# Performance work log

Measured on AMD Instinct MI355X. Metric: run time of the kernel, lower is better.

Reference implementation:

```python
import jax, jax.numpy as jnp
import numpy as np

B, F, A, U = 4096, 64, 8, 32  # batch, n_features, num_att, n_outputs
R = 2.0                       # the 'r' scaling inside exp(kernel * r)


def setup_inputs() -> dict:
    key = jax.random.key(0)
    k1, k2 = jax.random.split(key)
    inputs = jax.random.normal(k1, (B, F), dtype=jnp.float32)
    # per-exclusion-feature attention kernels, stacked: [F, A, F, U]
    limit = float(np.sqrt(6.0 / (F + U)))  # glorot_uniform
    kernels = jax.random.uniform(k2, (F, A, F, U), dtype=jnp.float32,
                                 minval=-limit, maxval=limit)
    return {"inputs": inputs, "kernels": kernels}


def reference(inputs, kernels):
    # inputs: [B, F]; kernels: [j=F excluded-feature index, A, F, U]
    f = inputs.shape[-1]
    mask = 1.0 - jnp.eye(f, dtype=inputs.dtype)          # [j, F]: zero out feature j
    xm = mask[:, None, :] * inputs[None, :, :]           # [j, B, F]
    z = jnp.einsum('jbf,jafu->jabu', xm, kernels)        # [j, A, B, U]
    z = jax.nn.softmax(z, axis=-1)                       # softmax over units
    w = jnp.exp(kernels * R)                             # [j, A, F, U]
    scores = jnp.einsum('jabu,jafu->jabf', z, w)         # [j, A, B, F]
    scores = scores.mean(axis=0)                         # mean over exclusion axis -> [A, B, F]
    return jax.nn.softmax(scores, axis=-1)               # [A, B, F]
```

## Files before the change

### kernel.cpp

```cpp
#include <hip/hip_runtime.h>
#include <hip/hip_bf16.h>
#include <math.h>

#define B_ 4096
#define F_ 64
#define A_ 8
#define U_ 32

typedef float f32x4 __attribute__((ext_vector_type(4)));
typedef short bf16x8 __attribute__((ext_vector_type(8)));

#define KD_OFF (4ull << 20)

static __device__ __forceinline__ unsigned int pk_bf16(float lo, float hi) {
    union { __hip_bfloat162 h2; unsigned int u; } cv;
    cv.h2 = __float22bfloat162_rn(make_float2(lo, hi));
    return cv.u;
}
static __device__ __forceinline__ float rb(float f) {
    unsigned int u = __float_as_uint(f);
    u += 0x7FFFu + ((u >> 16) & 1u);
    return __uint_as_float(u & 0xFFFF0000u);
}

__global__ __launch_bounds__(256) void ife_prep(const float* __restrict__ kern,
                                                unsigned char* __restrict__ ws)
{
    const int bid = blockIdx.x;
    const int a = bid >> 6, j = bid & 63;
    const int t = threadIdx.x;
    __shared__ float st[64][36];

    const float* src = kern + ((size_t)j * A_ + a) * (F_ * U_);
    {
        const int f = t >> 2, u0 = (t & 3) * 8;
        *(float4*)&st[f][u0]     = *(const float4*)&src[f * U_ + u0];
        *(float4*)&st[f][u0 + 4] = *(const float4*)&src[f * U_ + u0 + 4];
    }
    __syncthreads();

    unsigned char* dst = ws + (size_t)bid * 8192;
    const int fragid = t >> 6, lane = t & 63, q = lane >> 4, c = lane & 15;

    {
        const int kc = fragid >> 1, ut = fragid & 1;
        const int f0 = kc * 32 + q * 8, u = ut * 16 + c;
        unsigned int w[4];
        #pragma unroll
        for (int i = 0; i < 4; ++i)
            w[i] = pk_bf16(st[f0 + 2 * i][u], st[f0 + 2 * i + 1][u]);
        *(uint4*)(dst + fragid * 1024 + lane * 16) = make_uint4(w[0], w[1], w[2], w[3]);
    }
    {
        const int f = fragid * 16 + c, u0 = q * 8;
        const float4 wa = *(const float4*)&st[f][u0];
        const float4 wb = *(const float4*)&st[f][u0 + 4];
        unsigned int w[4];
        w[0] = pk_bf16(__expf(2.f * wa.x), __expf(2.f * wa.y));
        w[1] = pk_bf16(__expf(2.f * wa.z), __expf(2.f * wa.w));
        w[2] = pk_bf16(__expf(2.f * wb.x), __expf(2.f * wb.y));
        w[3] = pk_bf16(__expf(2.f * wb.z), __expf(2.f * wb.w));
        *(uint4*)(dst + 4096 + fragid * 1024 + lane * 16) = make_uint4(w[0], w[1], w[2], w[3]);
    }
    if (t < U_)
        ((float*)(ws + KD_OFF))[(size_t)bid * U_ + t] = rb(st[j][t]);
}

__global__ __launch_bounds__(256, 2) void ife_main(const float* __restrict__ x,
                                                   const unsigned char* __restrict__ ws,
                                                   float* __restrict__ out)
{
    const int a = blockIdx.y, bt = blockIdx.x, t = threadIdx.x;
    const int wv = t >> 6, lane = t & 63, q = lane >> 4, c = lane & 15;

    __shared__ float Xf[64][66];
    __shared__ float Kd[64][32];
    __shared__ __align__(16) unsigned int PbufA[4][16][20];
    __shared__ __align__(16) unsigned int PbufB[4][16][20];

    bf16x8 Xh[2];
    {
        const float* xr = x + (size_t)(bt * 64 + wv * 16 + c) * F_;
        #pragma unroll
        for (int kc = 0; kc < 2; ++kc) {
            const float4 va = *(const float4*)&xr[kc * 32 + q * 8];
            const float4 vb = *(const float4*)&xr[kc * 32 + q * 8 + 4];
            union { unsigned int u[4]; bf16x8 v; } H;
            H.u[0] = pk_bf16(va.x, va.y);
            H.u[1] = pk_bf16(va.z, va.w);
            H.u[2] = pk_bf16(vb.x, vb.y);
            H.u[3] = pk_bf16(vb.z, vb.w);
            Xh[kc] = H.v;
        }
    }
    {
        const int row = t >> 2, cb = (t & 3) * 16;
        const float* xsrc = x + (size_t)(bt * 64 + row) * F_ + cb;
        #pragma unroll
        for (int i = 0; i < 16; i += 4) {
            const float4 v = *(const float4*)&xsrc[i];
            Xf[row][cb + i]     = rb(v.x);
            Xf[row][cb + i + 1] = rb(v.y);
            Xf[row][cb + i + 2] = rb(v.z);
            Xf[row][cb + i + 3] = rb(v.w);
        }
    }
    {
        const float* kd = (const float*)(ws + KD_OFF) + (size_t)a * 64 * U_;
        const int jj = t >> 2, u0 = (t & 3) * 8;
        *(float4*)&Kd[jj][u0]     = *(const float4*)&kd[jj * U_ + u0];
        *(float4*)&Kd[jj][u0 + 4] = *(const float4*)&kd[jj * U_ + u0 + 4];
    }
    __syncthreads();

    const unsigned int psel = (q < 2) ? 0x05040100u : 0x07060302u;
    const unsigned char* fbase = ws + (size_t)a * 64 * 8192 + (size_t)lane * 16;

    union { unsigned int u[4]; bf16x8 v; } oc;
    oc.u[0] = 0x3F803F80u; oc.u[1] = 0x3F803F80u; oc.u[2] = 0x3F803F80u; oc.u[3] = 0x3F803F80u;
    const bf16x8 ONES = oc.v;
    const f32x4 vzero = (f32x4){0.f, 0.f, 0.f, 0.f};

    f32x4 S0 = vzero, S1 = vzero, S2 = vzero, S3 = vzero;

    bf16x8 KA[4], WA[4], KB[4], WB[4];
    float xjA[4], xjB[4], kdA0, kdA1, kdB0, kdB1;
    uint4 ra0, ra1, rb0, rb1;

    auto LOADF = [&](bf16x8* K, bf16x8* W, int jj) {
        const unsigned char* p = fbase + (size_t)jj * 8192;
        #pragma unroll
        for (int i = 0; i < 4; ++i) {
            K[i] = *(const bf16x8*)(p + i * 1024);
            W[i] = *(const bf16x8*)(p + 4096 + i * 1024);
        }
    };

    auto SCAL = [&](float* xj, float& k0, float& k1, int j) {
        #pragma unroll
        for (int r = 0; r < 4; ++r) xj[r] = Xf[wv * 16 + q * 4 + r][j];
        k0 = Kd[j][c];
        k1 = Kd[j][16 + c];
    };

    auto ZW = [&](const bf16x8* K, const float* xj, float kd0, float kd1,
                  unsigned int (*P)[16][20]) {
        f32x4 ZA = vzero, ZB = vzero;
        ZA = __builtin_amdgcn_mfma_f32_16x16x32_bf16(Xh[0], K[0], ZA, 0, 0, 0);
        ZA = __builtin_amdgcn_mfma_f32_16x16x32_bf16(Xh[1], K[2], ZA, 0, 0, 0);
        ZB = __builtin_amdgcn_mfma_f32_16x16x32_bf16(Xh[0], K[1], ZB, 0, 0, 0);
        ZB = __builtin_amdgcn_mfma_f32_16x16x32_bf16(Xh[1], K[3], ZB, 0, 0, 0);
        #pragma unroll
        for (int r = 0; r < 4; ++r) {
            const float e0 = __expf(ZA[r] - xj[r] * kd0);
            const float e1 = __expf(ZB[r] - xj[r] * kd1);
            P[wv][q * 4 + r][c] = pk_bf16(e0, e1);
        }
    };

    auto RD = [&](uint4& pa, uint4& pb, const unsigned int (*P)[16][20]) {
        asm volatile("" ::: "memory");
        pa = *(const uint4*)&P[wv][c][(q & 1) * 8];
        pb = *(const uint4*)&P[wv][c][(q & 1) * 8 + 4];
    };

    auto FN = [&](const uint4& pa, const uint4& pb, const bf16x8* W) {
        union { unsigned int u[4]; bf16x8 v; } E;
        E.u[0] = __builtin_amdgcn_perm(pa.y, pa.x, psel);
        E.u[1] = __builtin_amdgcn_perm(pa.w, pa.z, psel);
        E.u[2] = __builtin_amdgcn_perm(pb.y, pb.x, psel);
        E.u[3] = __builtin_amdgcn_perm(pb.w, pb.z, psel);

        const f32x4 sv = __builtin_amdgcn_mfma_f32_16x16x32_bf16(E.v, ONES, vzero, 0, 0, 0);
        f32x4 D0 = __builtin_amdgcn_mfma_f32_16x16x32_bf16(E.v, W[0], vzero, 0, 0, 0);
        f32x4 D1 = __builtin_amdgcn_mfma_f32_16x16x32_bf16(E.v, W[1], vzero, 0, 0, 0);
        f32x4 D2 = __builtin_amdgcn_mfma_f32_16x16x32_bf16(E.v, W[2], vzero, 0, 0, 0);
        f32x4 D3 = __builtin_amdgcn_mfma_f32_16x16x32_bf16(E.v, W[3], vzero, 0, 0, 0);
        #pragma unroll
        for (int r = 0; r < 4; ++r) {
            const float inv = __builtin_amdgcn_rcpf(sv[r]);
            S0[r] += D0[r] * inv;
            S1[r] += D1[r] * inv;
            S2[r] += D2[r] * inv;
            S3[r] += D3[r] * inv;
        }
    };

    LOADF(KA, WA, 0);
    SCAL(xjA, kdA0, kdA1, 0);
    ZW(KA, xjA, kdA0, kdA1, PbufA);
    LOADF(KB, WB, 1);
    SCAL(xjB, kdB0, kdB1, 1);

    for (int j = 0; j < 62; j += 2) {
        RD(ra0, ra1, PbufA);
        ZW(KB, xjB, kdB0, kdB1, PbufB);
        FN(ra0, ra1, WA);
        LOADF(KA, WA, j + 2);
        SCAL(xjA, kdA0, kdA1, j + 2);
        RD(rb0, rb1, PbufB);
        ZW(KA, xjA, kdA0, kdA1, PbufA);
        FN(rb0, rb1, WB);
        LOADF(KB, WB, j + 3);
        SCAL(xjB, kdB0, kdB1, j + 3);
    }
    RD(ra0, ra1, PbufA);
    ZW(KB, xjB, kdB0, kdB1, PbufB);
    FN(ra0, ra1, WA);
    RD(rb0, rb1, PbufB);
    FN(rb0, rb1, WB);

    const float sc = 1.f / 64.f;
    #pragma unroll
    for (int r = 0; r < 4; ++r) {
        const float e0 = __expf(S0[r] * sc);
        const float e1 = __expf(S1[r] * sc);
        const float e2 = __expf(S2[r] * sc);
        const float e3 = __expf(S3[r] * sc);
        float s = e0 + e1 + e2 + e3;
        s += __shfl_xor(s, 1);
        s += __shfl_xor(s, 2);
        s += __shfl_xor(s, 4);
        s += __shfl_xor(s, 8);
        const float inv = 1.f / s;
        const int b = bt * 64 + wv * 16 + q * 4 + r;
        float* o = out + ((size_t)a * B_ + b) * F_ + c;
        o[0]  = e0 * inv;
        o[16] = e1 * inv;
        o[32] = e2 * inv;
        o[48] = e3 * inv;
    }
}

extern "C" void kernel_launch(void* const* d_in, const int* in_sizes, int n_in,
                              void* d_out, int out_size, void* d_ws, size_t ws_size,
                              hipStream_t stream) {
    (void)in_sizes; (void)n_in; (void)out_size; (void)ws_size;
    const float* x    = (const float*)d_in[0];
    const float* kern = (const float*)d_in[1];
    float* out        = (float*)d_out;
    unsigned char* ws = (unsigned char*)d_ws;

    hipLaunchKernelGGL(ife_prep, dim3(F_ * A_), dim3(256), 0, stream, kern, ws);
    hipLaunchKernelGGL(ife_main, dim3(B_ / 64, A_), dim3(256), 0, stream, x, ws, out);
}
```

Measured before the change: 97.35 us.

## Split exclusion-axis loop across two wave groups with shared-memory reduction

New measurement: 157.8 us. 1.62x slower.

```diff
diff --git a/kernel.cpp b/kernel.cpp
--- a/kernel.cpp
+++ b/kernel.cpp
@@ -66,21 +66,21 @@
         ((float*)(ws + KD_OFF))[(size_t)bid * U_ + t] = rb(st[j][t]);
 }
 
-__global__ __launch_bounds__(256, 2) void ife_main(const float* __restrict__ x,
+__global__ __launch_bounds__(512, 4) void ife_main(const float* __restrict__ x,
                                                    const unsigned char* __restrict__ ws,
                                                    float* __restrict__ out)
 {
     const int a = blockIdx.y, bt = blockIdx.x, t = threadIdx.x;
     const int wv = t >> 6, lane = t & 63, q = lane >> 4, c = lane & 15;
+    const int grp = wv >> 2, w4 = wv & 3;
 
     __shared__ float Xf[64][66];
     __shared__ float Kd[64][32];
-    __shared__ __align__(16) unsigned int PbufA[4][16][20];
-    __shared__ __align__(16) unsigned int PbufB[4][16][20];
+    __shared__ __align__(16) unsigned int Pbuf[2][8][16][20];
 
     bf16x8 Xh[2];
     {
-        const float* xr = x + (size_t)(bt * 64 + wv * 16 + c) * F_;
+        const float* xr = x + (size_t)(bt * 64 + w4 * 16 + c) * F_;
         #pragma unroll
         for (int kc = 0; kc < 2; ++kc) {
             const float4 va = *(const float4*)&xr[kc * 32 + q * 8];
@@ -94,22 +94,19 @@
         }
     }
     {
-        const int row = t >> 2, cb = (t & 3) * 16;
+        const int row = t >> 3, cb = (t & 7) * 8;
         const float* xsrc = x + (size_t)(bt * 64 + row) * F_ + cb;
-        #pragma unroll
-        for (int i = 0; i < 16; i += 4) {
-            const float4 v = *(const float4*)&xsrc[i];
-            Xf[row][cb + i]     = rb(v.x);
-            Xf[row][cb + i + 1] = rb(v.y);
-            Xf[row][cb + i + 2] = rb(v.z);
-            Xf[row][cb + i + 3] = rb(v.w);
-        }
+        const float4 v0 = *(const float4*)&xsrc[0];
+        const float4 v1 = *(const float4*)&xsrc[4];
+        Xf[row][cb + 0] = rb(v0.x); Xf[row][cb + 1] = rb(v0.y);
+        Xf[row][cb + 2] = rb(v0.z); Xf[row][cb + 3] = rb(v0.w);
+        Xf[row][cb + 4] = rb(v1.x); Xf[row][cb + 5] = rb(v1.y);
+        Xf[row][cb + 6] = rb(v1.z); Xf[row][cb + 7] = rb(v1.w);
     }
     {
         const float* kd = (const float*)(ws + KD_OFF) + (size_t)a * 64 * U_;
-        const int jj = t >> 2, u0 = (t & 3) * 8;
-        *(float4*)&Kd[jj][u0]     = *(const float4*)&kd[jj * U_ + u0];
-        *(float4*)&Kd[jj][u0 + 4] = *(const float4*)&kd[jj * U_ + u0 + 4];
+        const int jj = t >> 3, u0 = (t & 7) * 4;
+        *(float4*)&Kd[jj][u0] = *(const float4*)&kd[jj * U_ + u0];
     }
     __syncthreads();
 
@@ -138,7 +135,7 @@
 
     auto SCAL = [&](float* xj, float& k0, float& k1, int j) {
         #pragma unroll
-        for (int r = 0; r < 4; ++r) xj[r] = Xf[wv * 16 + q * 4 + r][j];
+        for (int r = 0; r < 4; ++r) xj[r] = Xf[w4 * 16 + q * 4 + r][j];
         k0 = Kd[j][c];
         k1 = Kd[j][16 + c];
     };
@@ -162,6 +159,7 @@
         asm volatile("" ::: "memory");
         pa = *(const uint4*)&P[wv][c][(q & 1) * 8];
         pb = *(const uint4*)&P[wv][c][(q & 1) * 8 + 4];
+        asm volatile("" ::: "memory");
     };
 
     auto FN = [&](const uint4& pa, const uint4& pb, const bf16x8* W) {
@@ -186,49 +184,68 @@
         }
     };
 
-    LOADF(KA, WA, 0);
-    SCAL(xjA, kdA0, kdA1, 0);
-    ZW(KA, xjA, kdA0, kdA1, PbufA);
-    LOADF(KB, WB, 1);
-    SCAL(xjB, kdB0, kdB1, 1);
-
-    for (int j = 0; j < 62; j += 2) {
-        RD(ra0, ra1, PbufA);
-        ZW(KB, xjB, kdB0, kdB1, PbufB);
+    const int jb = grp * 32;
+    LOADF(KA, WA, jb);
+    SCAL(xjA, kdA0, kdA1, jb);
+    ZW(KA, xjA, kdA0, kdA1, Pbuf[0]);
+    LOADF(KB, WB, jb + 1);
+    SCAL(xjB, kdB0, kdB1, jb + 1);
+
+    for (int j = 0; j < 30; j += 2) {
+        RD(ra0, ra1, Pbuf[0]);
+        ZW(KB, xjB, kdB0, kdB1, Pbuf[1]);
         FN(ra0, ra1, WA);
-        LOADF(KA, WA, j + 2);
-        SCAL(xjA, kdA0, kdA1, j + 2);
-        RD(rb0, rb1, PbufB);
-        ZW(KA, xjA, kdA0, kdA1, PbufA);
+        LOADF(KA, WA, jb + j + 2);
+        SCAL(xjA, kdA0, kdA1, jb + j + 2);
+        RD(rb0, rb1, Pbuf[1]);
+        ZW(KA, xjA, kdA0, kdA1, Pbuf[0]);
         FN(rb0, rb1, WB);
-        LOADF(KB, WB, j + 3);
-        SCAL(xjB, kdB0, kdB1, j + 3);
-    }
-    RD(ra0, ra1, PbufA);
-    ZW(KB, xjB, kdB0, kdB1, PbufB);
+        LOADF(KB, WB, jb + j + 3);
+        SCAL(xjB, kdB0, kdB1, jb + j + 3);
+    }
+    RD(ra0, ra1, Pbuf[0]);
+    ZW(KB, xjB, kdB0, kdB1, Pbuf[1]);
     FN(ra0, ra1, WA);
-    RD(rb0, rb1, PbufB);
+    RD(rb0, rb1, Pbuf[1]);
     FN(rb0, rb1, WB);
 
-    const float sc = 1.f / 64.f;
-    #pragma unroll
-    for (int r = 0; r < 4; ++r) {
-        const float e0 = __expf(S0[r] * sc);
-        const float e1 = __expf(S1[r] * sc);
-        const float e2 = __expf(S2[r] * sc);
-        const float e3 = __expf(S3[r] * sc);
-        float s = e0 + e1 + e2 + e3;
-        s += __shfl_xor(s, 1);
-        s += __shfl_xor(s, 2);
-        s += __shfl_xor(s, 4);
-        s += __shfl_xor(s, 8);
-        const float inv = 1.f / s;
-        const int b = bt * 64 + wv * 16 + q * 4 + r;
-        float* o = out + ((size_t)a * B_ + b) * F_ + c;
-        o[0]  = e0 * inv;
-        o[16] = e1 * inv;
-        o[32] = e2 * inv;
-        o[48] = e3 * inv;
+    __syncthreads();
+    float* Sred = (float*)Pbuf;
+    if (grp == 1) {
+        float* p = Sred + (size_t)(w4 * 64 + lane) * 20;
+        *(f32x4*)(p + 0)  = S0;
+        *(f32x4*)(p + 4)  = S1;
+        *(f32x4*)(p + 8)  = S2;
+        *(f32x4*)(p + 12) = S3;
+    }
+    __syncthreads();
+    if (grp == 0) {
+        const float* p = Sred + (size_t)(w4 * 64 + lane) * 20;
+        S0 += *(const f32x4*)(p + 0);
+        S1 += *(const f32x4*)(p + 4);
+        S2 += *(const f32x4*)(p + 8);
+        S3 += *(const f32x4*)(p + 12);
+
+        const float sc = 1.f / 64.f;
+        #pragma unroll
+        for (int r = 0; r < 4; ++r) {
+            const float e0 = __expf(S0[r] * sc);
+            const float e1 = __expf(S1[r] * sc);
+            const float e2 = __expf(S2[r] * sc);
+            const float e3 = __expf(S3[r] * sc);
+            float s = e0 + e1 + e2 + e3;
+            s += __shfl_xor(s, 1);
+            s += __shfl_xor(s, 2);
+            s += __shfl_xor(s, 4);
+            s += __shfl_xor(s, 8);
+            const float inv = 1.f / s;
+            const int b = bt * 64 + w4 * 16 + q * 4 + r;
+            float* o = out + ((size_t)a * B_ + b) * F_ + c;
+            o[0]  = e0 * inv;
+            o[16] = e1 * inv;
+            o[32] = e2 * inv;
+            o[48] = e3 * inv;
+        }
     }
 }
 
@@ -242,5 +259,5 @@
     unsigned char* ws = (unsigned char*)d_ws;
 
     hipLaunchKernelGGL(ife_prep, dim3(F_ * A_), dim3(256), 0, stream, kern, ws);
-    hipLaunchKernelGGL(ife_main, dim3(B_ / 64, A_), dim3(256), 0, stream, x, ws, out);
-}
+    hipLaunchKernelGGL(ife_main, dim3(B_ / 64, A_), dim3(512), 0, stream, x, ws, out);
+}
```
